# Performance work log

Hardware: AMD Instinct MI355X
Metric: run time of the kernel (lower is better)

Reference implementation:

```python
import jax, jax.numpy as jnp
import numpy as np

N = 8192      # points
NOBJ = 8      # objects
H = 64        # hidden_size (required by channel arithmetic, see notes)
CDIM = 128
K = 20
KNN = 360
EPS = 1e-5


def _lrelu(x):
    return jnp.where(x >= 0, x, 0.2 * x)


def _inorm2d(x):  # x: [C, N, K]; InstanceNorm2d, affine=False, biased var
    m = x.mean(axis=(1, 2), keepdims=True)
    v = ((x - m) ** 2).mean(axis=(1, 2), keepdims=True)
    return (x - m) / jnp.sqrt(v + EPS)


def _inorm1d(x):  # x: [C, L]
    m = x.mean(axis=1, keepdims=True)
    v = ((x - m) ** 2).mean(axis=1, keepdims=True)
    return (x - m) / jnp.sqrt(v + EPS)


def _block2d(W, f):  # 1x1 conv (no bias) + InstanceNorm2d + LeakyReLU(0.2)
    return _lrelu(_inorm2d(jnp.einsum('oc,cnk->onk', W, f)))


def _block1d(W, f):
    return _lrelu(_inorm1d(W @ f))


def _edge_feat(xc, idx):  # xc: [C, N], idx: [N, k] -> [2C, N, k]
    xt = xc.T                                   # [N, C]
    nb = xt[idx]                                # [N, k, C] gather
    ctr = jnp.broadcast_to(xt[:, None, :], nb.shape)
    return jnp.concatenate([nb - ctr, ctr], axis=2).transpose(2, 0, 1)


def _knn_idx(x, tag, k):  # kNN within same node_tag, self excluded
    xs = jax.lax.stop_gradient(x)
    sq = jnp.sum(xs * xs, axis=1)
    d2 = sq[:, None] + sq[None, :] - 2.0 * (xs @ xs.T)
    valid = (tag[:, None] == tag[None, :]) & ~jnp.eye(xs.shape[0], dtype=bool)
    d2 = jnp.where(valid, d2, jnp.inf)
    _, idx = jax.lax.top_k(-d2, k)              # ascending distance order
    return idx


def setup_inputs() -> dict:
    key = jax.random.key(0)
    ks = jax.random.split(key, 16)
    x = jax.random.normal(ks[0], (N, 3), dtype=jnp.float32)
    node_tag = (jnp.arange(N, dtype=jnp.int32) // (N // NOBJ))  # equal groups

    def w(k, o, i):
        return jax.random.normal(k, (o, i), dtype=jnp.float32) * (1.0 / np.sqrt(i))

    return {
        'x': x, 'node_tag': node_tag, 'n_obj': NOBJ,
        'W1': w(ks[1], H, 6),       'W2': w(ks[2], H, H),
        'W3': w(ks[3], H, 2 * H),   'W4': w(ks[4], H, H),
        'W5': w(ks[5], H, 2 * H),   'W6': w(ks[6], H, H),
        'W7': w(ks[7], H, 2 * H),   'W8': w(ks[8], H, H),
        'W9': w(ks[9], 128, 4 * H),
        'W10': w(ks[10], 2 * H, 3 * H),
        'W11': w(ks[11], 2 * H, 3 * H),
        'W12': w(ks[12], H, 3 * H),
        'W13': w(ks[13], H, 2 * H),
        'Wr': w(ks[14], CDIM, H),
    }


def reference(x, node_tag, n_obj, W1, W2, W3, W4, W5, W6, W7, W8, W9, W10,
              W11, W12, W13, Wr):
    n = x.shape[0]
    idx = _knn_idx(x, node_tag, KNN)            # [N, 360]

    f = _edge_feat(x.T, idx[:, :K])             # [6, N, 20]
    x1 = _block2d(W2, _block2d(W1, f)).max(axis=-1)            # [H, N]
    f = _edge_feat(x1, idx[:, :40:2])
    x2 = _block2d(W4, _block2d(W3, f)).max(axis=-1) + x1
    f = _edge_feat(x2, idx[:, :120:6])
    x3 = _block2d(W6, _block2d(W5, f)).max(axis=-1) + x2
    f = _edge_feat(x3, idx[:, :360:18])
    x4 = _block2d(W8, _block2d(W7, f)).max(axis=-1) + x3

    g = _block1d(W9, jnp.concatenate([x1, x2, x3, x4], axis=0))  # [128, N]
    g = jnp.broadcast_to(g.max(axis=1, keepdims=True), (128, n))

    x4 = _block1d(W10, jnp.concatenate([g, x4], axis=0))   # [2H, N]
    x3 = _block1d(W11, jnp.concatenate([x4, x3], axis=0))  # [2H, N]
    x2 = _block1d(W12, jnp.concatenate([x3, x2], axis=0))  # [H, N]
    x1 = _block1d(W13, jnp.concatenate([x2, x1], axis=0))  # [H, N]

    code = (Wr @ x1).T                                     # [N, c_dim]
    tag = node_tag.astype(jnp.int32)
    sums = jax.ops.segment_sum(code, tag, num_segments=n_obj)
    cnt = jax.ops.segment_sum(jnp.ones((n,), code.dtype), tag,
                              num_segments=n_obj)
    return sums / jnp.maximum(cnt, 1.0)[:, None]           # [n_obj, c_dim]
```

## Files before the change

### kernel.cpp

```cpp
#include <hip/hip_runtime.h>
#include <hip/hip_bf16.h>
#include <stdint.h>

typedef __hip_bfloat16 bf16;
typedef __attribute__((ext_vector_type(8))) short bfrag;
typedef __attribute__((ext_vector_type(4))) short s16x4;
typedef __attribute__((ext_vector_type(4))) float f32x4;

#define NPTS 8192
#define KSEL 20
#define MBIG (NPTS*KSEL)
#define EPSN 1e-5f

__device__ __forceinline__ float lrelu(float x){ return x >= 0.f ? x : 0.2f*x; }
__device__ __forceinline__ float ldx(const void* p, int i, int isbf){
  return isbf ? __bfloat162float(((const bf16*)p)[i]) : ((const float*)p)[i];
}
__device__ __forceinline__ short f2bs(float f){
  union { bf16 h; short s; } u;
  u.h = __float2bfloat16(f);
  return u.s;
}
__device__ __forceinline__ f32x4 mfma16(bfrag a, bfrag b, f32x4 c){
  return __builtin_amdgcn_mfma_f32_16x16x32_bf16(a, b, c, 0, 0, 0);
}
__device__ __forceinline__ unsigned fenc(float x){
  unsigned u = __float_as_uint(x);
  return (u & 0x80000000u) ? ~u : (u | 0x80000000u);
}
__device__ __forceinline__ float fdec(unsigned u){
  return __uint_as_float((u & 0x80000000u) ? (u & 0x7FFFFFFFu) : ~u);
}
__device__ __forceinline__ unsigned long long u64min(unsigned long long a, unsigned long long b){ return a<b?a:b; }
__device__ __forceinline__ unsigned long long u64max(unsigned long long a, unsigned long long b){ return a<b?b:a; }
__device__ __forceinline__ void ce(unsigned long long &a, unsigned long long &b, bool asc){
  unsigned long long mn = a<b?a:b, mx = a<b?b:a;
  a = asc ? mn : mx;
  b = asc ? mx : mn;
}

__global__ void zero_kernel(float* __restrict__ p, int n){
  int i = blockIdx.x*256 + threadIdx.x;
  if (i < n) p[i] = 0.f;
}

__global__ void detect_kernel(const void* __restrict__ x, int* __restrict__ badf){
  int i = blockIdx.x*256 + threadIdx.x;
  int bad = 0;
  for (; i < NPTS*3; i += gridDim.x*256){
    float v = __bfloat162float(((const bf16*)x)[i]);
    if (!(fabsf(v) < 1000.0f)) bad = 1;
  }
  if (__any(bad) && (threadIdx.x & 63) == 0) atomicOr(badf, 1);
}

__global__ __launch_bounds__(256) void knn_kernel(const void* __restrict__ x,
                                                  const int* __restrict__ tag,
                                                  int* __restrict__ idxc,
                                                  const int* __restrict__ flagp){
  __shared__ unsigned long long keysL[1024];
  const int isbf = (*flagp == 0);
  const int i = blockIdx.x;
  const int base = (i >> 10) << 10;
  const int t = threadIdx.x;
  const float xi = ldx(x, i*3+0, isbf);
  const float yi = ldx(x, i*3+1, isbf);
  const float zi = ldx(x, i*3+2, isbf);
  const float sqi = xi*xi + yi*yi + zi*zi;
  const int tagi = tag[i];

  unsigned long long v[4];
  #pragma unroll
  for (int r = 0; r < 4; r++){
    int j = 4*t + r, gj = base + j;
    float xj = ldx(x, gj*3+0, isbf);
    float yj = ldx(x, gj*3+1, isbf);
    float zj = ldx(x, gj*3+2, isbf);
    float sqj = xj*xj + yj*yj + zj*zj;
    float dot = xi*xj + yi*yj + zi*zj;
    float d2 = sqi + sqj - 2.0f*dot;
    bool valid = (gj != i) && (tag[gj] == tagi);
    unsigned k = valid ? fenc(d2) : 0xFFFFFFFFu;
    v[r] = ((unsigned long long)k << 32) | (unsigned)gj;
  }

  #pragma unroll
  for (int ksz = 2; ksz <= 1024; ksz <<= 1){
    #pragma unroll
    for (int jj = ksz >> 1; jj > 0; jj >>= 1){
      if (jj >= 256){
        __syncthreads();
        keysL[4*t+0] = v[0]; keysL[4*t+1] = v[1];
        keysL[4*t+2] = v[2]; keysL[4*t+3] = v[3];
        __syncthreads();
        const int pt = t ^ (jj >> 2);
        const bool keep_min = (((t & (ksz >> 2)) == 0) == ((t & (jj >> 2)) == 0));
        #pragma unroll
        for (int r = 0; r < 4; r++){
          unsigned long long o = keysL[4*pt + r];
          v[r] = keep_min ? u64min(v[r], o) : u64max(v[r], o);
        }
      } else if (jj >= 4){
        const int mask = jj >> 2;
        const bool keep_min = (((t & (ksz >> 2)) == 0) == ((t & mask) == 0));
        #pragma unroll
        for (int r = 0; r < 4; r++){
          unsigned long long o = __shfl_xor(v[r], mask, 64);
          v[r] = keep_min ? u64min(v[r], o) : u64max(v[r], o);
        }
      } else if (jj == 2){
        const bool asc = ((t & (ksz >> 2)) == 0);
        ce(v[0], v[2], asc);
        ce(v[1], v[3], asc);
      } else {
        if (ksz == 2){
          ce(v[0], v[1], true);
          ce(v[2], v[3], false);
        } else {
          const bool asc = ((t & (ksz >> 2)) == 0);
          ce(v[0], v[1], asc);
          ce(v[2], v[3], asc);
        }
      }
    }
  }

  __syncthreads();
  keysL[4*t+0] = v[0]; keysL[4*t+1] = v[1];
  keysL[4*t+2] = v[2]; keysL[4*t+3] = v[3];
  __syncthreads();
  if (t < 80){
    int s = t / 20, k = t - s*20;
    int step = (s == 0) ? 1 : (s == 1) ? 2 : (s == 2) ? 6 : 18;
    idxc[i*80 + t] = (int)(keysL[k*step] & 0xFFFFFFFFu);
  }
}

__global__ __launch_bounds__(256) void pq3_kernel(
    const void* __restrict__ xin, const void* __restrict__ Wc,
    float* __restrict__ Pt, float* __restrict__ Qt,
    const int* __restrict__ flagp)
{
  __shared__ float WaS[16][3], WdS[16][3];
  const int isbf = (*flagp == 0);
  const int t = threadIdx.x;
  const int n0 = (blockIdx.x & 31) * 256;
  const int cg = (blockIdx.x >> 5) * 16;
  if (t < 48){
    int r = t / 3, k = t - r*3;
    float wa = ldx(Wc, (cg + r)*6 + k, isbf);
    float wb = ldx(Wc, (cg + r)*6 + 3 + k, isbf);
    WaS[r][k] = wa; WdS[r][k] = wb - wa;
  }
  __syncthreads();
  const int n = n0 + t;
  float xr[3];
  #pragma unroll
  for (int k = 0; k < 3; k++) xr[k] = ldx(xin, n*3 + k, isbf);
  float pv[16], qv[16];
  #pragma unroll
  for (int r = 0; r < 16; r++){
    float p = 0.f, q = 0.f;
    #pragma unroll
    for (int k = 0; k < 3; k++){
      p += WaS[r][k] * xr[k];
      q += WdS[r][k] * xr[k];
    }
    pv[r] = p; qv[r] = q;
  }
  #pragma unroll
  for (int r4 = 0; r4 < 4; r4++){
    *(float4*)&Pt[n*64 + cg + r4*4] = make_float4(pv[r4*4], pv[r4*4+1], pv[r4*4+2], pv[r4*4+3]);
    *(float4*)&Qt[n*64 + cg + r4*4] = make_float4(qv[r4*4], qv[r4*4+1], qv[r4*4+2], qv[r4*4+3]);
  }
}

__global__ __launch_bounds__(256) void pqm_kernel(
    const float* __restrict__ rmaxp,
    const void* __restrict__ Wc,
    const float* __restrict__ straw,
    const float* __restrict__ resid,
    float* __restrict__ Pt, float* __restrict__ Qt,
    float* __restrict__ xout,
    const int* __restrict__ flagp)
{
  __shared__ __align__(16) short Fs[32][72];
  __shared__ float nm[64], niv[64];
  const int isbf = (*flagp == 0);
  const int t = threadIdx.x;
  const int n0 = blockIdx.x * 32;
  const int lane = t & 63, w = t >> 6;
  const int nn = lane & 15, quad = lane >> 4;

  if (t < 64){
    const float invMB = 1.0f/(float)MBIG;
    float m = straw[t] * invMB;
    float vv = straw[256+t]*invMB - m*m;
    nm[t] = m;
    niv[t] = 1.0f / sqrtf(fmaxf(vv, 0.f) + EPSN);
  }

  bfrag ap0, ap1, aq0, aq1;
  {
    const int row = 16*w + nn;
    #pragma unroll
    for (int j = 0; j < 8; j++){
      float wa0 = ldx(Wc, row*128 +      quad*8 + j, isbf);
      float wa1 = ldx(Wc, row*128 + 32 + quad*8 + j, isbf);
      float wb0 = ldx(Wc, row*128 + 64 + quad*8 + j, isbf);
      float wb1 = ldx(Wc, row*128 + 96 + quad*8 + j, isbf);
      ap0[j] = f2bs(wa0); ap1[j] = f2bs(wa1);
      aq0[j] = f2bs(wb0 - wa0); aq1[j] = f2bs(wb1 - wa1);
    }
  }
  __syncthreads();

  {
    const int jc = t & 31, kg = t >> 5;
    const int n = n0 + jc;
    #pragma unroll
    for (int u = 0; u < 2; u++){
      s16x4 pk;
      #pragma unroll
      for (int z = 0; z < 4; z++){
        int k = kg*8 + u*4 + z;
        float rv = rmaxp[k*NPTS + n];
        float vx = lrelu((rv - nm[k]) * niv[k]) + (resid ? resid[k*NPTS + n] : 0.f);
        xout[k*NPTS + n] = vx;
        pk[z] = f2bs(vx);
      }
      *(s16x4*)&Fs[jc][kg*8 + u*4] = pk;
    }
  }
  __syncthreads();

  #pragma unroll
  for (int q = 0; q < 2; q++){
    bfrag b0 = *(bfrag*)&Fs[q*16 + nn][quad*8];
    bfrag b1 = *(bfrag*)&Fs[q*16 + nn][32 + quad*8];
    f32x4 accp = {0.f,0.f,0.f,0.f}, accq = {0.f,0.f,0.f,0.f};
    accp = mfma16(ap0, b0, accp); accp = mfma16(ap1, b1, accp);
    accq = mfma16(aq0, b0, accq); accq = mfma16(aq1, b1, accq);
    int n = n0 + q*16 + nn;
    int c0 = 16*w + quad*4;
    *(float4*)&Pt[n*64 + c0] = make_float4(accp[0], accp[1], accp[2], accp[3]);
    *(float4*)&Qt[n*64 + c0] = make_float4(accq[0], accq[1], accq[2], accq[3]);
  }
}

__global__ __launch_bounds__(256) void stats1_kernel(
    const float* __restrict__ Pt, const float* __restrict__ Qt,
    const int* __restrict__ idxc, int sidx, float* __restrict__ stats)
{
  __shared__ __align__(16) float Qs[1024];
  __shared__ int ids[320];
  const int t = threadIdx.x;
  const int n0 = blockIdx.x * 16;
  for (int l = t; l < 1024; l += 256) Qs[l] = Qt[n0*64 + l];
  for (int l = t; l < 320; l += 256){
    int p = l / 20, k = l - p*20;
    ids[l] = idxc[(n0+p)*80 + sidx*20 + k] & (NPTS-1);
  }
  __syncthreads();
  const int tx = t & 15, ty = t >> 4;
  const int kq = tx >> 2, p0 = (tx & 3)*4;
  float sacc[4] = {0,0,0,0}, qacc[4] = {0,0,0,0};
  #pragma unroll
  for (int s = 0; s < 5; s++){
    int k = s*4 + kq;
    #pragma unroll
    for (int j = 0; j < 4; j++){
      int p = p0 + j;
      int nb = ids[p*20 + k];
      float4 pvv = *(const float4*)&Pt[nb*64 + ty*4];
      float4 qvv = *(const float4*)&Qs[p*64 + ty*4];
      float e0 = pvv.x+qvv.x, e1 = pvv.y+qvv.y, e2 = pvv.z+qvv.z, e3 = pvv.w+qvv.w;
      sacc[0]+=e0; sacc[1]+=e1; sacc[2]+=e2; sacc[3]+=e3;
      qacc[0]+=e0*e0; qacc[1]+=e1*e1; qacc[2]+=e2*e2; qacc[3]+=e3*e3;
    }
  }
  #pragma unroll
  for (int i = 0; i < 4; i++){
    float s = sacc[i], q = qacc[i];
    #pragma unroll
    for (int off = 8; off; off >>= 1){
      s += __shfl_down(s, off, 16);
      q += __shfl_down(q, off, 16);
    }
    if (tx == 0){
      atomicAdd(&stats[ty*4+i], s);
      atomicAdd(&stats[256+ty*4+i], q);
    }
  }
}

__global__ __launch_bounds__(256) void conv2_kernel(
    const float* __restrict__ Pt, const float* __restrict__ Qt,
    const int* __restrict__ idxc, int sidx,
    const void* __restrict__ W2c,
    const float* __restrict__ st1raw,
    float* __restrict__ stats2,
    float* __restrict__ rawmax,
    const int* __restrict__ flagp)
{
  __shared__ __align__(16) short Gs[64][72];
  __shared__ __align__(16) float Qs[1024];
  __shared__ int ids[320];
  __shared__ float nm1[64], niv1[64];
  const int isbf = (*flagp == 0);
  const int t = threadIdx.x;
  const int n0 = blockIdx.x * 16;
  const float invMB = 1.0f/(float)MBIG;

  for (int l = t; l < 1024; l += 256) Qs[l] = Qt[n0*64 + l];
  for (int l = t; l < 320; l += 256){
    int p = l / 20, k = l - p*20;
    ids[l] = idxc[(n0+p)*80 + sidx*20 + k] & (NPTS-1);
  }
  if (t < 64){
    float m = st1raw[t] * invMB;
    float v = st1raw[256+t]*invMB - m*m;
    nm1[t] = m;
    niv1[t] = 1.0f / sqrtf(fmaxf(v, 0.f) + EPSN);
  }

  const int lane = t & 63, w = t >> 6;
  const int nn = lane & 15, quad = lane >> 4;
  bfrag af0, af1;
  #pragma unroll
  for (int j = 0; j < 8; j++){
    af0[j] = f2bs(ldx(W2c, (16*w + nn)*64 +      quad*8 + j, isbf));
    af1[j] = f2bs(ldx(W2c, (16*w + nn)*64 + 32 + quad*8 + j, isbf));
  }
  __syncthreads();

  const int tx = t & 15, ty = t >> 4;
  float sacc[4] = {0,0,0,0}, qacc[4] = {0,0,0,0};
  float mxr[4] = {-3.4e38f,-3.4e38f,-3.4e38f,-3.4e38f};

  for (int s = 0; s < 5; s++){
    #pragma unroll
    for (int j = 0; j < 4; j++){
      int cg = tx*4 + j;
      int q = cg >> 4, p = cg & 15;
      int nb = ids[p*20 + s*4 + q];
      float4 pvv = *(const float4*)&Pt[nb*64 + ty*4];
      float4 qvv = *(const float4*)&Qs[p*64 + ty*4];
      s16x4 gv;
      gv[0] = f2bs(lrelu((pvv.x+qvv.x - nm1[ty*4+0]) * niv1[ty*4+0]));
      gv[1] = f2bs(lrelu((pvv.y+qvv.y - nm1[ty*4+1]) * niv1[ty*4+1]));
      gv[2] = f2bs(lrelu((pvv.z+qvv.z - nm1[ty*4+2]) * niv1[ty*4+2]));
      gv[3] = f2bs(lrelu((pvv.w+qvv.w - nm1[ty*4+3]) * niv1[ty*4+3]));
      *(s16x4*)&Gs[cg][ty*4] = gv;
    }
    __syncthreads();
    #pragma unroll
    for (int q = 0; q < 4; q++){
      bfrag b0 = *(bfrag*)&Gs[q*16 + nn][quad*8];
      bfrag b1 = *(bfrag*)&Gs[q*16 + nn][32 + quad*8];
      f32x4 acc = {0.f, 0.f, 0.f, 0.f};
      acc = mfma16(af0, b0, acc);
      acc = mfma16(af1, b1, acc);
      #pragma unroll
      for (int r = 0; r < 4; r++){
        float v = acc[r];
        sacc[r] += v; qacc[r] += v*v;
        mxr[r] = fmaxf(mxr[r], v);
      }
    }
    __syncthreads();
  }

  #pragma unroll
  for (int r = 0; r < 4; r++){
    int rr = 16*w + quad*4 + r;
    float s = sacc[r], q2 = qacc[r];
    #pragma unroll
    for (int off = 8; off; off >>= 1){
      s  += __shfl_down(s, off, 16);
      q2 += __shfl_down(q2, off, 16);
    }
    if (nn == 0){
      atomicAdd(&stats2[rr], s);
      atomicAdd(&stats2[256+rr], q2);
    }
    rawmax[rr*NPTS + n0 + nn] = mxr[r];
  }
}

__global__ __launch_bounds__(256) void maxres_kernel(
    const float* __restrict__ rawmax, const float* __restrict__ st2raw,
    const float* __restrict__ resid, float* __restrict__ xout)
{
  const float invMB = 1.0f/(float)MBIG;
  int g = blockIdx.x*256 + threadIdx.x;
  int c = g >> 13;
  float m = st2raw[c] * invMB;
  float v = st2raw[256+c]*invMB - m*m;
  float iv = 1.0f / sqrtf(fmaxf(v, 0.f) + EPSN);
  float y = lrelu((rawmax[g] - m) * iv);
  xout[g] = y + (resid ? resid[g] : 0.f);
}

template<int CTOT>
__global__ __launch_bounds__(256) void gemm1d_kernel(
    const void* __restrict__ W, int ldw, int koffW,
    const float* __restrict__ A, const float* __restrict__ Araw, float invA, int CA,
    const float* __restrict__ B,
    const float* __restrict__ cvec,
    float* __restrict__ Y,
    float* __restrict__ stats, unsigned* __restrict__ maxenc,
    const int* __restrict__ flagp)
{
  __shared__ __align__(16) short Fs[64][72];
  __shared__ float am[256], aiv[256];
  const int t = threadIdx.x;
  const int isbf = (*flagp == 0);
  const int colbase = (blockIdx.x & 127) * 64;
  const int rb = (blockIdx.x >> 7) * 64;
  const int lane = t & 63, w = t >> 6;
  const int nn = lane & 15, quad = lane >> 4;

  if (Araw && t < CA){
    float m = Araw[t]*invA;
    float v = Araw[256+t]*invA - m*m;
    am[t] = m; aiv[t] = 1.0f/sqrtf(fmaxf(v,0.f)+EPSN);
  }

  constexpr int K32 = CTOT >> 5;
  bfrag af[K32];
  const int arow = rb + 16*w + nn;
  #pragma unroll
  for (int f = 0; f < K32; f++)
    #pragma unroll
    for (int j = 0; j < 8; j++)
      af[f][j] = f2bs(ldx(W, arow*ldw + koffW + f*32 + quad*8 + j, isbf));

  f32x4 acc[4] = {};
  const int jcol = t & 63, kg = t >> 6;

  for (int kc = 0; kc < CTOT; kc += 64){
    __syncthreads();
    #pragma unroll
    for (int u = 0; u < 4; u++){
      int kl = kg*16 + u*4;
      s16x4 pk;
      #pragma unroll
      for (int z = 0; z < 4; z++){
        int k = kc + kl + z;
        float v;
        if (k < CA){
          v = A[k*NPTS + colbase + jcol];
          if (Araw) v = lrelu((v - am[k]) * aiv[k]);
        } else {
          v = B[(k-CA)*NPTS + colbase + jcol];
        }
        pk[z] = f2bs(v);
      }
      *(s16x4*)&Fs[jcol][kl] = pk;
    }
    __syncthreads();
    const int f0 = kc >> 5;
    #pragma unroll
    for (int q = 0; q < 4; q++){
      bfrag b0 = *(bfrag*)&Fs[q*16+nn][quad*8];
      bfrag b1 = *(bfrag*)&Fs[q*16+nn][32 + quad*8];
      acc[q] = mfma16(af[f0],   b0, acc[q]);
      acc[q] = mfma16(af[f0+1], b1, acc[q]);
    }
  }

  #pragma unroll
  for (int r = 0; r < 4; r++){
    int rr = rb + 16*w + quad*4 + r;
    float cv = cvec ? cvec[rr] : 0.f;
    float sum = 0.f, q2 = 0.f, mxv = -3.4e38f;
    #pragma unroll
    for (int q = 0; q < 4; q++){
      float v = acc[q][r] + cv;
      sum += v; q2 += v*v; mxv = fmaxf(mxv, v);
      if (Y) Y[rr*NPTS + colbase + q*16 + nn] = v;
    }
    #pragma unroll
    for (int off = 8; off; off >>= 1){
      sum += __shfl_down(sum, off, 16);
      q2  += __shfl_down(q2, off, 16);
      mxv  = fmaxf(mxv, __shfl_down(mxv, off, 16));
    }
    if (nn == 0){
      atomicAdd(&stats[rr], sum);
      atomicAdd(&stats[256+rr], q2);
      if (maxenc) atomicMax(&maxenc[rr], fenc(mxv));
    }
  }
}

__global__ void finalize_g_kernel(float* __restrict__ statsG,
    unsigned* __restrict__ gmaxenc, float* __restrict__ c0,
    const void* __restrict__ W10, const int* __restrict__ flagp)
{
  __shared__ float gsh[128];
  const int isbf = (*flagp == 0);
  int c = threadIdx.x;
  if (c < 128){
    float m = statsG[c] * (1.f/NPTS);
    float v = statsG[256+c]*(1.f/NPTS) - m*m;
    float iv = 1.0f / sqrtf(fmaxf(v, 0.f) + EPSN);
    gsh[c] = lrelu((fdec(gmaxenc[c]) - m) * iv);
  }
  __syncthreads();
  if (c < 128){
    float s = 0.f;
    for (int j = 0; j < 128; j++) s += ldx(W10, c*192 + j, isbf) * gsh[j];
    c0[c] = s;
  }
}

__global__ __launch_bounds__(256) void segsum_kernel(
    const float* __restrict__ ybuf, const float* __restrict__ straw,
    const int* __restrict__ tag, float* __restrict__ seg, float* __restrict__ cnt)
{
  const float invMN = 1.0f/(float)NPTS;
  int g = blockIdx.x*256 + threadIdx.x;
  int c = g >> 13, n = g & (NPTS-1);
  float m = straw[c] * invMN;
  float vv = straw[256+c]*invMN - m*m;
  float iv = 1.0f / sqrtf(fmaxf(vv, 0.f) + EPSN);
  float v = lrelu((ybuf[c*NPTS + n] - m) * iv);
  int tg = tag[n] & 7;
  int lane = threadIdx.x & 63;
  int t0 = __shfl(tg, 0, 64);
  bool uni = __all(tg == t0);
  if (uni){
    #pragma unroll
    for (int off = 32; off; off >>= 1) v += __shfl_down(v, off, 64);
    if (lane == 0){
      atomicAdd(&seg[t0*64 + c], v);
      if (c == 0) atomicAdd(cnt + t0, 64.f);
    }
  } else {
    atomicAdd(&seg[tg*64 + c], v);
    if (c == 0) atomicAdd(cnt + tg, 1.f);
  }
}

__global__ void final_kernel(const void* __restrict__ Wr,
    const float* __restrict__ seg, const float* __restrict__ cnt,
    void* __restrict__ out, int total, const int* __restrict__ flagp)
{
  const int isbf = (*flagp == 0);
  int q = blockIdx.x*blockDim.x + threadIdx.x;
  if (q >= total) return;
  int g = q >> 7, c = q & 127;
  float s = 0.f;
  for (int j = 0; j < 64; j++) s += ldx(Wr, c*64 + j, isbf) * seg[g*64 + j];
  float r = s / fmaxf(cnt[g], 1.f);
  if (isbf) ((bf16*)out)[q] = __float2bfloat16(r);
  else      ((float*)out)[q] = r;
}

extern "C" void kernel_launch(void* const* d_in, const int* in_sizes, int n_in,
                              void* d_out, int out_size, void* d_ws, size_t ws_size,
                              hipStream_t stream)
{
  const void* x   = d_in[0];
  const int* tag  = (const int*)d_in[1];
  const void* W1  = d_in[3];
  const void* W2  = d_in[4];
  const void* W3  = d_in[5];
  const void* W4  = d_in[6];
  const void* W5  = d_in[7];
  const void* W6  = d_in[8];
  const void* W7  = d_in[9];
  const void* W8  = d_in[10];
  const void* W9  = d_in[11];
  const void* W10 = d_in[12];
  const void* W11 = d_in[13];
  const void* W12 = d_in[14];
  const void* W13 = d_in[15];
  const void* Wr  = d_in[16];

  char* ws = (char*)d_ws;
  int*      idxc = (int*)ws;
  float*    xs   = (float*)(ws + 2621440);
  float* x1 = xs;
  float* x2 = xs +  64*NPTS;
  float* x3 = xs + 128*NPTS;
  float* x4 = xs + 192*NPTS;
  float*    y0   = (float*)(ws + 11010048);
  float*    y1   = (float*)(ws + 15204352);
  float*    rmax = (float*)(ws + 19398656);
  float*    Pt   = y0;
  float*    Qt   = y0 + 64*NPTS;
  float*    st   = (float*)(ws + 21495808);
  auto L = [&](int l){ return st + l*1024; };
  int*      flag     = (int*)(st + 13312);
  unsigned* gmaxenc  = (unsigned*)(st + 13440);
  float*    c0v      = st + 13568;
  float*    seg      = st + 13824;
  float*    cnt      = seg + 512;

  zero_kernel<<<64, 256, 0, stream>>>(st, 16384);
  detect_kernel<<<12, 256, 0, stream>>>(x, flag);
  knn_kernel<<<NPTS, 256, 0, stream>>>(x, tag, idxc, flag);

  pq3_kernel<<<128, 256, 0, stream>>>(x, W1, Pt, Qt, flag);
  stats1_kernel<<<512, 256, 0, stream>>>(Pt, Qt, idxc, 0, L(0));
  conv2_kernel<<<512, 256, 0, stream>>>(Pt, Qt, idxc, 0, W2, L(0), L(1), rmax, flag);
  pqm_kernel<<<256, 256, 0, stream>>>(rmax, W3, L(1), nullptr, Pt, Qt, x1, flag);
  stats1_kernel<<<512, 256, 0, stream>>>(Pt, Qt, idxc, 1, L(2));
  conv2_kernel<<<512, 256, 0, stream>>>(Pt, Qt, idxc, 1, W4, L(2), L(3), rmax, flag);
  pqm_kernel<<<256, 256, 0, stream>>>(rmax, W5, L(3), x1, Pt, Qt, x2, flag);
  stats1_kernel<<<512, 256, 0, stream>>>(Pt, Qt, idxc, 2, L(4));
  conv2_kernel<<<512, 256, 0, stream>>>(Pt, Qt, idxc, 2, W6, L(4), L(5), rmax, flag);
  pqm_kernel<<<256, 256, 0, stream>>>(rmax, W7, L(5), x2, Pt, Qt, x3, flag);
  stats1_kernel<<<512, 256, 0, stream>>>(Pt, Qt, idxc, 3, L(6));
  conv2_kernel<<<512, 256, 0, stream>>>(Pt, Qt, idxc, 3, W8, L(6), L(7), rmax, flag);
  maxres_kernel<<<64*NPTS/256, 256, 0, stream>>>(rmax, L(7), x3, x4);

  gemm1d_kernel<256><<<256, 256, 0, stream>>>(W9, 256, 0, xs, nullptr, 0.f, 256,
                                              nullptr, nullptr, nullptr, L(8), gmaxenc, flag);
  finalize_g_kernel<<<1, 128, 0, stream>>>(L(8), gmaxenc, c0v, W10, flag);

  const float invMN = 1.0f/(float)NPTS;
  gemm1d_kernel<64> <<<256, 256, 0, stream>>>(W10, 192, 128, nullptr, nullptr, 0.f, 0,
                                              x4, c0v, y0, L(9), nullptr, flag);
  gemm1d_kernel<192><<<256, 256, 0, stream>>>(W11, 192, 0, y0, L(9), invMN, 128,
                                              x3, nullptr, y1, L(10), nullptr, flag);
  gemm1d_kernel<192><<<128, 256, 0, stream>>>(W12, 192, 0, y1, L(10), invMN, 128,
                                              x2, nullptr, y0, L(11), nullptr, flag);
  gemm1d_kernel<128><<<128, 256, 0, stream>>>(W13, 128, 0, y0, L(11), invMN, 64,
                                              x1, nullptr, y1, L(12), nullptr, flag);

  segsum_kernel<<<64*NPTS/256, 256, 0, stream>>>(y1, L(12), tag, seg, cnt);
  final_kernel<<<4, 256, 0, stream>>>(Wr, seg, cnt, d_out, out_size, flag);
}
```

Before: 886.8 us.

## Split stats gather across k halves, prefetch conv2 gathers, widen small GEMM grids

stats1 now splits each 16-point tile's 20 neighbours into two blocks of 10, doubling the grid to raise parallelism for the gather-bound statistics pass. conv2 software-prefetches the next step's neighbour gathers into registers while the current step is converted and multiplied, and drops one barrier per iteration. gemm1d gains a column-tile template parameter so the W12/W13 layers launch 256 blocks with 32-column tiles instead of 128. The changes add register pressure in conv2 and more atomics in stats1.

```diff
diff --git a/kernel.cpp b/kernel.cpp
--- a/kernel.cpp
+++ b/kernel.cpp
@@ -253,30 +253,34 @@
     const int* __restrict__ idxc, int sidx, float* __restrict__ stats)
 {
   __shared__ __align__(16) float Qs[1024];
-  __shared__ int ids[320];
+  __shared__ int ids[160];
   const int t = threadIdx.x;
-  const int n0 = blockIdx.x * 16;
+  const int tile = blockIdx.x >> 1;
+  const int kb = (blockIdx.x & 1) * 10;
+  const int n0 = tile * 16;
   for (int l = t; l < 1024; l += 256) Qs[l] = Qt[n0*64 + l];
-  for (int l = t; l < 320; l += 256){
-    int p = l / 20, k = l - p*20;
-    ids[l] = idxc[(n0+p)*80 + sidx*20 + k] & (NPTS-1);
+  if (t < 160){
+    int p = t / 10, kk = t - p*10;
+    ids[t] = idxc[(n0+p)*80 + sidx*20 + kb + kk] & (NPTS-1);
   }
   __syncthreads();
   const int tx = t & 15, ty = t >> 4;
   const int kq = tx >> 2, p0 = (tx & 3)*4;
   float sacc[4] = {0,0,0,0}, qacc[4] = {0,0,0,0};
   #pragma unroll
-  for (int s = 0; s < 5; s++){
-    int k = s*4 + kq;
-    #pragma unroll
-    for (int j = 0; j < 4; j++){
-      int p = p0 + j;
-      int nb = ids[p*20 + k];
-      float4 pvv = *(const float4*)&Pt[nb*64 + ty*4];
-      float4 qvv = *(const float4*)&Qs[p*64 + ty*4];
-      float e0 = pvv.x+qvv.x, e1 = pvv.y+qvv.y, e2 = pvv.z+qvv.z, e3 = pvv.w+qvv.w;
-      sacc[0]+=e0; sacc[1]+=e1; sacc[2]+=e2; sacc[3]+=e3;
-      qacc[0]+=e0*e0; qacc[1]+=e1*e1; qacc[2]+=e2*e2; qacc[3]+=e3*e3;
+  for (int s = 0; s < 3; s++){
+    int kk = s*4 + kq;
+    if (kk < 10){
+      #pragma unroll
+      for (int j = 0; j < 4; j++){
+        int p = p0 + j;
+        int nb = ids[p*10 + kk];
+        float4 pvv = *(const float4*)&Pt[nb*64 + ty*4];
+        float4 qvv = *(const float4*)&Qs[p*64 + ty*4];
+        float e0 = pvv.x+qvv.x, e1 = pvv.y+qvv.y, e2 = pvv.z+qvv.z, e3 = pvv.w+qvv.w;
+        sacc[0]+=e0; sacc[1]+=e1; sacc[2]+=e2; sacc[3]+=e3;
+        qacc[0]+=e0*e0; qacc[1]+=e1*e1; qacc[2]+=e2*e2; qacc[3]+=e3*e3;
+      }
     }
   }
   #pragma unroll
@@ -338,20 +342,36 @@
   float sacc[4] = {0,0,0,0}, qacc[4] = {0,0,0,0};
   float mxr[4] = {-3.4e38f,-3.4e38f,-3.4e38f,-3.4e38f};
 
+  float4 ep[4];
+  #pragma unroll
+  for (int j = 0; j < 4; j++){
+    int cg = tx*4 + j;
+    int q = cg >> 4, p = cg & 15;
+    ep[j] = *(const float4*)&Pt[ids[p*20 + q]*64 + ty*4];
+  }
+
   for (int s = 0; s < 5; s++){
+    if (s) __syncthreads();
     #pragma unroll
     for (int j = 0; j < 4; j++){
       int cg = tx*4 + j;
-      int q = cg >> 4, p = cg & 15;
-      int nb = ids[p*20 + s*4 + q];
-      float4 pvv = *(const float4*)&Pt[nb*64 + ty*4];
+      int p = cg & 15;
       float4 qvv = *(const float4*)&Qs[p*64 + ty*4];
       s16x4 gv;
-      gv[0] = f2bs(lrelu((pvv.x+qvv.x - nm1[ty*4+0]) * niv1[ty*4+0]));
-      gv[1] = f2bs(lrelu((pvv.y+qvv.y - nm1[ty*4+1]) * niv1[ty*4+1]));
-      gv[2] = f2bs(lrelu((pvv.z+qvv.z - nm1[ty*4+2]) * niv1[ty*4+2]));
-      gv[3] = f2bs(lrelu((pvv.w+qvv.w - nm1[ty*4+3]) * niv1[ty*4+3]));
+      gv[0] = f2bs(lrelu((ep[j].x+qvv.x - nm1[ty*4+0]) * niv1[ty*4+0]));
+      gv[1] = f2bs(lrelu((ep[j].y+qvv.y - nm1[ty*4+1]) * niv1[ty*4+1]));
+      gv[2] = f2bs(lrelu((ep[j].z+qvv.z - nm1[ty*4+2]) * niv1[ty*4+2]));
+      gv[3] = f2bs(lrelu((ep[j].w+qvv.w - nm1[ty*4+3]) * niv1[ty*4+3]));
       *(s16x4*)&Gs[cg][ty*4] = gv;
+    }
+    float4 ep2[4];
+    if (s < 4){
+      #pragma unroll
+      for (int j = 0; j < 4; j++){
+        int cg = tx*4 + j;
+        int q = cg >> 4, p = cg & 15;
+        ep2[j] = *(const float4*)&Pt[ids[p*20 + (s+1)*4 + q]*64 + ty*4];
+      }
     }
     __syncthreads();
     #pragma unroll
@@ -368,7 +388,10 @@
         mxr[r] = fmaxf(mxr[r], v);
       }
     }
-    __syncthreads();
+    if (s < 4){
+      #pragma unroll
+      for (int j = 0; j < 4; j++) ep[j] = ep2[j];
+    }
   }
 
   #pragma unroll
@@ -402,7 +425,7 @@
   xout[g] = y + (resid ? resid[g] : 0.f);
 }
 
-template<int CTOT>
+template<int CTOT, int COLS>
 __global__ __launch_bounds__(256) void gemm1d_kernel(
     const void* __restrict__ W, int ldw, int koffW,
     const float* __restrict__ A, const float* __restrict__ Araw, float invA, int CA,
@@ -412,12 +435,13 @@
     float* __restrict__ stats, unsigned* __restrict__ maxenc,
     const int* __restrict__ flagp)
 {
-  __shared__ __align__(16) short Fs[64][72];
+  __shared__ __align__(16) short Fs[COLS][72];
   __shared__ float am[256], aiv[256];
   const int t = threadIdx.x;
   const int isbf = (*flagp == 0);
-  const int colbase = (blockIdx.x & 127) * 64;
-  const int rb = (blockIdx.x >> 7) * 64;
+  constexpr int NCT = NPTS / COLS;
+  const int colbase = (blockIdx.x % NCT) * COLS;
+  const int rb = (blockIdx.x / NCT) * 64;
   const int lane = t & 63, w = t >> 6;
   const int nn = lane & 15, quad = lane >> 4;
 
@@ -436,14 +460,16 @@
     for (int j = 0; j < 8; j++)
       af[f][j] = f2bs(ldx(W, arow*ldw + koffW + f*32 + quad*8 + j, isbf));
 
-  f32x4 acc[4] = {};
-  const int jcol = t & 63, kg = t >> 6;
+  constexpr int QN = COLS/16;
+  constexpr int UN = COLS/16;
+  f32x4 acc[QN] = {};
+  const int jcol = t % COLS, kg = t / COLS;
 
   for (int kc = 0; kc < CTOT; kc += 64){
     __syncthreads();
     #pragma unroll
-    for (int u = 0; u < 4; u++){
-      int kl = kg*16 + u*4;
+    for (int u = 0; u < UN; u++){
+      int kl = kg*(4*UN) + u*4;
       s16x4 pk;
       #pragma unroll
       for (int z = 0; z < 4; z++){
@@ -462,7 +488,7 @@
     __syncthreads();
     const int f0 = kc >> 5;
     #pragma unroll
-    for (int q = 0; q < 4; q++){
+    for (int q = 0; q < QN; q++){
       bfrag b0 = *(bfrag*)&Fs[q*16+nn][quad*8];
       bfrag b1 = *(bfrag*)&Fs[q*16+nn][32 + quad*8];
       acc[q] = mfma16(af[f0],   b0, acc[q]);
@@ -476,7 +502,7 @@
     float cv = cvec ? cvec[rr] : 0.f;
     float sum = 0.f, q2 = 0.f, mxv = -3.4e38f;
     #pragma unroll
-    for (int q = 0; q < 4; q++){
+    for (int q = 0; q < QN; q++){
       float v = acc[q][r] + cv;
       sum += v; q2 += v*v; mxv = fmaxf(mxv, v);
       if (Y) Y[rr*NPTS + colbase + q*16 + nn] = v;
@@ -605,32 +631,32 @@
   knn_kernel<<<NPTS, 256, 0, stream>>>(x, tag, idxc, flag);
 
   pq3_kernel<<<128, 256, 0, stream>>>(x, W1, Pt, Qt, flag);
-  stats1_kernel<<<512, 256, 0, stream>>>(Pt, Qt, idxc, 0, L(0));
+  stats1_kernel<<<1024, 256, 0, stream>>>(Pt, Qt, idxc, 0, L(0));
   conv2_kernel<<<512, 256, 0, stream>>>(Pt, Qt, idxc, 0, W2, L(0), L(1), rmax, flag);
   pqm_kernel<<<256, 256, 0, stream>>>(rmax, W3, L(1), nullptr, Pt, Qt, x1, flag);
-  stats1_kernel<<<512, 256, 0, stream>>>(Pt, Qt, idxc, 1, L(2));
+  stats1_kernel<<<1024, 256, 0, stream>>>(Pt, Qt, idxc, 1, L(2));
   conv2_kernel<<<512, 256, 0, stream>>>(Pt, Qt, idxc, 1, W4, L(2), L(3), rmax, flag);
   pqm_kernel<<<256, 256, 0, stream>>>(rmax, W5, L(3), x1, Pt, Qt, x2, flag);
-  stats1_kernel<<<512, 256, 0, stream>>>(Pt, Qt, idxc, 2, L(4));
+  stats1_kernel<<<1024, 256, 0, stream>>>(Pt, Qt, idxc, 2, L(4));
   conv2_kernel<<<512, 256, 0, stream>>>(Pt, Qt, idxc, 2, W6, L(4), L(5), rmax, flag);
   pqm_kernel<<<256, 256, 0, stream>>>(rmax, W7, L(5), x2, Pt, Qt, x3, flag);
-  stats1_kernel<<<512, 256, 0, stream>>>(Pt, Qt, idxc, 3, L(6));
+  stats1_kernel<<<1024, 256, 0, stream>>>(Pt, Qt, idxc, 3, L(6));
   conv2_kernel<<<512, 256, 0, stream>>>(Pt, Qt, idxc, 3, W8, L(6), L(7), rmax, flag);
   maxres_kernel<<<64*NPTS/256, 256, 0, stream>>>(rmax, L(7), x3, x4);
 
-  gemm1d_kernel<256><<<256, 256, 0, stream>>>(W9, 256, 0, xs, nullptr, 0.f, 256,
-                                              nullptr, nullptr, nullptr, L(8), gmaxenc, flag);
+  gemm1d_kernel<256,64><<<256, 256, 0, stream>>>(W9, 256, 0, xs, nullptr, 0.f, 256,
+                                                 nullptr, nullptr, nullptr, L(8), gmaxenc, flag);
   finalize_g_kernel<<<1, 128, 0, stream>>>(L(8), gmaxenc, c0v, W10, flag);
 
   const float invMN = 1.0f/(float)NPTS;
-  gemm1d_kernel<64> <<<256, 256, 0, stream>>>(W10, 192, 128, nullptr, nullptr, 0.f, 0,
-                                              x4, c0v, y0, L(9), nullptr, flag);
-  gemm1d_kernel<192><<<256, 256, 0, stream>>>(W11, 192, 0, y0, L(9), invMN, 128,
-                                              x3, nullptr, y1, L(10), nullptr, flag);
-  gemm1d_kernel<192><<<128, 256, 0, stream>>>(W12, 192, 0, y1, L(10), invMN, 128,
-                                              x2, nullptr, y0, L(11), nullptr, flag);
-  gemm1d_kernel<128><<<128, 256, 0, stream>>>(W13, 128, 0, y0, L(11), invMN, 64,
-                                              x1, nullptr, y1, L(12), nullptr, flag);
+  gemm1d_kernel<64,64> <<<256, 256, 0, stream>>>(W10, 192, 128, nullptr, nullptr, 0.f, 0,
+                                                 x4, c0v, y0, L(9), nullptr, flag);
+  gemm1d_kernel<192,64><<<256, 256, 0, stream>>>(W11, 192, 0, y0, L(9), invMN, 128,
+                                                 x3, nullptr, y1, L(10), nullptr, flag);
+  gemm1d_kernel<192,32><<<256, 256, 0, stream>>>(W12, 192, 0, y1, L(10), invMN, 128,
+                                                 x2, nullptr, y0, L(11), nullptr, flag);
+  gemm1d_kernel<128,32><<<256, 256, 0, stream>>>(W13, 128, 0, y0, L(11), invMN, 64,
+                                                 x1, nullptr, y1, L(12), nullptr, flag);
 
   segsum_kernel<<<64*NPTS/256, 256, 0, stream>>>(y1, L(12), tag, seg, cnt);
   final_kernel<<<4, 256, 0, stream>>>(Wr, seg, cnt, d_out, out_size, flag);
```

New measurement: 1.098 ms. 23.8% more time.
